# Kernel tuning notes

Hardware: AMD Instinct MI355X
Metric: run time of the kernel (lower is better)

The kernel has to match this reference:

```python
import jax, jax.numpy as jnp
import numpy as np

EMBED_DIM = 256
SEQ_LEN = 4096
BATCH = 8
ALPHA = 0.99


def setup_inputs() -> dict:
    key = jax.random.key(0)
    k_x, k_w, k_b = jax.random.split(key, 3)
    x = jax.random.normal(k_x, (BATCH, SEQ_LEN, EMBED_DIM), dtype=jnp.float32)
    # nn.Linear(embed_dim, 3*embed_dim): store as [d, 3d] so y = x @ Wqkv + bqkv
    Wqkv = jax.random.normal(k_w, (EMBED_DIM, 3 * EMBED_DIM), dtype=jnp.float32) * (EMBED_DIM ** -0.5)
    bqkv = jax.random.normal(k_b, (3 * EMBED_DIM,), dtype=jnp.float32) * 0.02
    return {"x": x, "Wqkv": Wqkv, "bqkv": bqkv}


def reference(x, Wqkv, bqkv):
    bs, sl, d = x.shape
    qkv = x @ Wqkv + bqkv                      # [bs, sl, 3d]
    q, k, v = jnp.split(qkv, 3, axis=-1)       # each [bs, sl, d]
    # causal * exponential-decay mask: M[i, j] = alpha**(i-j) for j <= i else 0
    i = jnp.arange(sl, dtype=jnp.float32)
    M = jnp.where(i[:, None] >= i[None, :],
                  jnp.power(jnp.float32(ALPHA), i[:, None] - i[None, :]),
                  0.0)                          # [sl, sl]
    scores = jnp.einsum('bqd,bkd->bqk', q, k) / jnp.sqrt(jnp.float32(d))
    out = jnp.einsum('bqk,bkd->bqd', scores * M, v)
    return out
```

## Files before the change

kernel.cpp:

```cpp
#include <hip/hip_runtime.h>

typedef __bf16 bf16x8 __attribute__((ext_vector_type(8)));
typedef float f32x4 __attribute__((ext_vector_type(4)));
typedef unsigned short u16;
typedef unsigned int u32;
typedef u16 u16x4 __attribute__((ext_vector_type(4)));
typedef u16 u16x8 __attribute__((ext_vector_type(8)));

#define L2ALPHA (-0.014499569f)

static __device__ __forceinline__ u16 f2bf(float f) {
    u32 u = __builtin_bit_cast(u32, f);
    return (u16)((u + 0x7FFFu + ((u >> 16) & 1u)) >> 16);
}

static __device__ __forceinline__ void gl2lds16(const void* g, void* l) {
    __builtin_amdgcn_global_load_lds(
        (const __attribute__((address_space(1))) u32*)g,
        (__attribute__((address_space(3))) u32*)l, 16, 0, 0);
}

__global__ __launch_bounds__(256, 2) void proj_kernel(
        const float* __restrict__ x, const float* __restrict__ Wq,
        const float* __restrict__ bias,
        u16* __restrict__ qb, u16* __restrict__ kb, u16* __restrict__ vb)
{
    __shared__ __align__(16) u16 Bs[32 * 128 * 8];
    __shared__ __align__(16) u16 As[4][32 * 40];

    const int tid = threadIdx.x, lane = tid & 63, w = tid >> 6;
    const int l = blockIdx.x;
    const int nb = l % 6;
    const int mt = l / 6;
    const int m0 = mt * 128, n0 = nb * 128;
    const int m = lane & 15, quad = lane >> 4;

    {
        const int col = tid & 127;
        const int khalf = tid >> 7;
        #pragma unroll
        for (int s = 0; s < 32; ++s) {
            int k0 = (khalf + 2 * s) * 4;
            u16x4 h;
            #pragma unroll
            for (int i = 0; i < 4; ++i)
                h[i] = f2bf(Wq[(k0 + i) * 768 + n0 + col]);
            *(u16x4*)&Bs[((k0 >> 3) * 128 + col) * 8 + (k0 & 7)] = h;
        }
    }
    __syncthreads();

    const int r = lane & 31, h = lane >> 5;
    const float* xrow = x + (size_t)(m0 + w * 32 + r) * 256 + h * 16;
    u16* As_w = &As[w][0];

    f32x4 acc[2][8];
    #pragma unroll
    for (int rt = 0; rt < 2; ++rt)
        #pragma unroll
        for (int ct = 0; ct < 8; ++ct)
            acc[rt][ct] = f32x4{0.f, 0.f, 0.f, 0.f};

    float4 g0 = *(const float4*)(xrow + 0);
    float4 g1 = *(const float4*)(xrow + 4);
    float4 g2 = *(const float4*)(xrow + 8);
    float4 g3 = *(const float4*)(xrow + 12);

    for (int kt = 0; kt < 8; ++kt) {
        u16x8 ha, hb;
        ha[0]=f2bf(g0.x); ha[1]=f2bf(g0.y); ha[2]=f2bf(g0.z); ha[3]=f2bf(g0.w);
        ha[4]=f2bf(g1.x); ha[5]=f2bf(g1.y); ha[6]=f2bf(g1.z); ha[7]=f2bf(g1.w);
        hb[0]=f2bf(g2.x); hb[1]=f2bf(g2.y); hb[2]=f2bf(g2.z); hb[3]=f2bf(g2.w);
        hb[4]=f2bf(g3.x); hb[5]=f2bf(g3.y); hb[6]=f2bf(g3.z); hb[7]=f2bf(g3.w);
        *(u16x8*)&As_w[r * 40 + h * 16]     = ha;
        *(u16x8*)&As_w[r * 40 + h * 16 + 8] = hb;

        if (kt < 7) {
            const float* xn = xrow + (kt + 1) * 32;
            g0 = *(const float4*)(xn + 0);
            g1 = *(const float4*)(xn + 4);
            g2 = *(const float4*)(xn + 8);
            g3 = *(const float4*)(xn + 12);
        }

        asm volatile("s_waitcnt lgkmcnt(0)" ::: "memory");

        bf16x8 af[2], bfr[8];
        #pragma unroll
        for (int rt = 0; rt < 2; ++rt)
            af[rt] = *(const bf16x8*)&As_w[(rt * 16 + m) * 40 + quad * 8];
        #pragma unroll
        for (int ct = 0; ct < 8; ++ct)
            bfr[ct] = *(const bf16x8*)&Bs[((kt * 4 + quad) * 128 + ct * 16 + m) * 8];
        #pragma unroll
        for (int rt = 0; rt < 2; ++rt)
            #pragma unroll
            for (int ct = 0; ct < 8; ++ct)
                acc[rt][ct] = __builtin_amdgcn_mfma_f32_16x16x32_bf16(
                    af[rt], bfr[ct], acc[rt][ct], 0, 0, 0);
    }

    const int b = m0 >> 12;
    const int jbase = (m0 & 4095) + w * 32;
    const int d0 = (nb & 1) * 128;

    if (nb < 2) {
        #pragma unroll
        for (int rt = 0; rt < 2; ++rt)
            #pragma unroll
            for (int ct = 0; ct < 8; ++ct) {
                int coll = ct * 16 + m;
                float bv = bias[d0 + coll];
                #pragma unroll
                for (int rr = 0; rr < 4; ++rr) {
                    int row = m0 + w * 32 + rt * 16 + quad * 4 + rr;
                    qb[(size_t)row * 256 + d0 + coll] = f2bf((acc[rt][ct][rr] + bv) * 0.0625f);
                }
            }
    } else if (nb < 4) {
        #pragma unroll
        for (int rt = 0; rt < 2; ++rt)
            #pragma unroll
            for (int ct = 0; ct < 8; ++ct) {
                int d = d0 + ct * 16 + m;
                float bv = bias[256 + d];
                int k8 = d >> 5, qk = (d >> 3) & 3, e = d & 7;
                #pragma unroll
                for (int rr = 0; rr < 4; ++rr) {
                    int j = jbase + rt * 16 + quad * 4 + rr;
                    int jt = j >> 5, hh = (j >> 4) & 1, mk = j & 15;
                    kb[((((size_t)(b * 128 + jt) * 2 + hh) * 8 + k8) * 64 + qk * 16 + mk) * 8 + e]
                        = f2bf(acc[rt][ct][rr] + bv);
                }
            }
    } else {
        #pragma unroll
        for (int rt = 0; rt < 2; ++rt)
            #pragma unroll
            for (int ct = 0; ct < 8; ++ct) {
                int d = d0 + ct * 16 + m;
                float bv = bias[512 + d];
                int dt = d >> 4, mv = d & 15;
                int j = jbase + rt * 16 + quad * 4;
                int jt = j >> 5, qv = (j >> 3) & 3, e0 = j & 7;
                u16x4 hv;
                #pragma unroll
                for (int rr = 0; rr < 4; ++rr) hv[rr] = f2bf(acc[rt][ct][rr] + bv);
                *(u16x4*)&vb[(((size_t)(b * 128 + jt) * 16 + dt) * 64 + qv * 16 + mv) * 8 + e0] = hv;
            }
    }
}

__global__ __launch_bounds__(256, 2) void attn_kernel(
        const u16* __restrict__ qb, const u16* __restrict__ kb,
        const u16* __restrict__ vb, float* __restrict__ out)
{
    __shared__ __align__(16) u16 Kf[2][8192];
    __shared__ __align__(16) u16 Vf[2][8192];
    __shared__ __align__(16) u16 Ps[4 * 32 * 40];

    const int tid = threadIdx.x, lane = tid & 63, w = tid >> 6;
    const int l = blockIdx.x;
    const int b = l & 7;
    const int m0 = (l >> 3) * 128;
    const int qrow0 = m0 + w * 32;
    const int m = lane & 15, quad = lane >> 4;
    const size_t rowbase = (size_t)b * 4096;

    bf16x8 qf[2][8];
    #pragma unroll
    for (int rg = 0; rg < 2; ++rg)
        #pragma unroll
        for (int k8 = 0; k8 < 8; ++k8)
            qf[rg][k8] = *(const bf16x8*)(qb + (rowbase + qrow0 + rg * 16 + m) * 256 + k8 * 32 + quad * 8);

    f32x4 acc[2][16];
    #pragma unroll
    for (int rg = 0; rg < 2; ++rg)
        #pragma unroll
        for (int dt = 0; dt < 16; ++dt)
            acc[rg][dt] = f32x4{0.f, 0.f, 0.f, 0.f};

    int t0 = (m0 - 1024) >> 5; if (t0 < 0) t0 = 0;
    const int t1 = (m0 >> 5) + 3;

    {
        const u16* kp = kb + (size_t)(b * 128 + t0) * 8192;
        const u16* vp = vb + (size_t)(b * 128 + t0) * 8192;
        #pragma unroll
        for (int s = 0; s < 4; ++s) {
            int c = tid + 256 * s;
            gl2lds16(kp + (size_t)c * 8, &Kf[0][c * 8]);
            gl2lds16(vp + (size_t)c * 8, &Vf[0][c * 8]);
        }
    }

    int p = 0;
    for (int t = t0; t <= t1; ++t) {
        __syncthreads();
        if (t < t1) {
            const u16* kp = kb + (size_t)(b * 128 + t + 1) * 8192;
            const u16* vp = vb + (size_t)(b * 128 + t + 1) * 8192;
            #pragma unroll
            for (int s = 0; s < 4; ++s) {
                int c = tid + 256 * s;
                gl2lds16(kp + (size_t)c * 8, &Kf[p ^ 1][c * 8]);
                gl2lds16(vp + (size_t)c * 8, &Vf[p ^ 1][c * 8]);
            }
        }
        const int j0 = t * 32;

        if (j0 <= qrow0 + 31 && j0 + 1055 >= qrow0) {
            f32x4 sA0{0.f,0.f,0.f,0.f}, sA1{0.f,0.f,0.f,0.f};
            f32x4 sB0{0.f,0.f,0.f,0.f}, sB1{0.f,0.f,0.f,0.f};
            #pragma unroll
            for (int k8 = 0; k8 < 8; ++k8) {
                bf16x8 bf0 = *(const bf16x8*)&Kf[p][(k8 * 64 + lane) * 8];
                sA0 = __builtin_amdgcn_mfma_f32_16x16x32_bf16(qf[0][k8], bf0, sA0, 0, 0, 0);
                sA1 = __builtin_amdgcn_mfma_f32_16x16x32_bf16(qf[1][k8], bf0, sA1, 0, 0, 0);
            }
            #pragma unroll
            for (int k8 = 0; k8 < 8; ++k8) {
                bf16x8 bf1 = *(const bf16x8*)&Kf[p][((8 + k8) * 64 + lane) * 8];
                sB0 = __builtin_amdgcn_mfma_f32_16x16x32_bf16(qf[0][k8], bf1, sB0, 0, 0, 0);
                sB1 = __builtin_amdgcn_mfma_f32_16x16x32_bf16(qf[1][k8], bf1, sB1, 0, 0, 0);
            }

            #pragma unroll
            for (int rg = 0; rg < 2; ++rg) {
                f32x4 sh0 = rg ? sA1 : sA0;
                f32x4 sh1 = rg ? sB1 : sB0;
                #pragma unroll
                for (int rr = 0; rr < 4; ++rr) {
                    int i = qrow0 + rg * 16 + quad * 4 + rr;
                    int dd0 = i - (j0 + m);
                    int dd1 = dd0 - 16;
                    float w0 = (dd0 >= 0) ? __builtin_amdgcn_exp2f((float)dd0 * L2ALPHA) : 0.0f;
                    float w1 = (dd1 >= 0) ? __builtin_amdgcn_exp2f((float)dd1 * L2ALPHA) : 0.0f;
                    int rowb = (w * 32 + rg * 16 + quad * 4 + rr) * 40;
                    Ps[rowb + m]      = f2bf(sh0[rr] * w0);
                    Ps[rowb + 16 + m] = f2bf(sh1[rr] * w1);
                }
            }
            asm volatile("s_waitcnt lgkmcnt(0)" ::: "memory");

            bf16x8 pa0 = *(const bf16x8*)&Ps[(w * 32 + m) * 40 + quad * 8];
            bf16x8 pa1 = *(const bf16x8*)&Ps[(w * 32 + 16 + m) * 40 + quad * 8];

            #pragma unroll
            for (int dt = 0; dt < 16; ++dt) {
                bf16x8 vf = *(const bf16x8*)&Vf[p][(dt * 64 + lane) * 8];
                acc[0][dt] = __builtin_amdgcn_mfma_f32_16x16x32_bf16(pa0, vf, acc[0][dt], 0, 0, 0);
                acc[1][dt] = __builtin_amdgcn_mfma_f32_16x16x32_bf16(pa1, vf, acc[1][dt], 0, 0, 0);
            }
        }
        p ^= 1;
    }

    #pragma unroll
    for (int rg = 0; rg < 2; ++rg)
        #pragma unroll
        for (int dt = 0; dt < 16; ++dt)
            #pragma unroll
            for (int rr = 0; rr < 4; ++rr)
                out[(rowbase + qrow0 + rg * 16 + quad * 4 + rr) * 256 + dt * 16 + m] = acc[rg][dt][rr];
}

extern "C" void kernel_launch(void* const* d_in, const int* in_sizes, int n_in,
                              void* d_out, int out_size, void* d_ws, size_t ws_size,
                              hipStream_t stream) {
    (void)in_sizes; (void)n_in; (void)out_size; (void)ws_size;
    const float* x    = (const float*)d_in[0];
    const float* Wq   = (const float*)d_in[1];
    const float* bias = (const float*)d_in[2];
    float* outp = (float*)d_out;

    const size_t per = (size_t)8 * 4096 * 256;
    u16* qb = (u16*)d_ws;
    u16* kb = qb + per;
    u16* vb = kb + per;

    proj_kernel<<<1536, 256, 0, stream>>>(x, Wq, bias, qb, kb, vb);
    attn_kernel<<<256, 256, 0, stream>>>(qb, kb, vb, outp);
}
```

Baseline: 197.0 us.

## Split KV tiles across two wave groups per block and reduce partial outputs

```diff
diff --git a/kernel.cpp b/kernel.cpp
--- a/kernel.cpp
+++ b/kernel.cpp
@@ -128,8 +128,8 @@
                 #pragma unroll
                 for (int rr = 0; rr < 4; ++rr) {
                     int j = jbase + rt * 16 + quad * 4 + rr;
-                    int jt = j >> 5, hh = (j >> 4) & 1, mk = j & 15;
-                    kb[((((size_t)(b * 128 + jt) * 2 + hh) * 8 + k8) * 64 + qk * 16 + mk) * 8 + e]
+                    int jt = j >> 5, jj = j & 31;
+                    kb[((((size_t)(b * 128 + jt) * 2 + (jj & 1)) * 8 + k8) * 64 + qk * 16 + (jj >> 1)) * 8 + e]
                         = f2bf(acc[rt][ct][rr] + bv);
                 }
             }
@@ -151,21 +151,22 @@
     }
 }
 
-__global__ __launch_bounds__(256, 2) void attn_kernel(
+__global__ __launch_bounds__(512, 2) void attn_kernel(
         const u16* __restrict__ qb, const u16* __restrict__ kb,
         const u16* __restrict__ vb, float* __restrict__ out)
 {
-    __shared__ __align__(16) u16 Kf[2][8192];
-    __shared__ __align__(16) u16 Vf[2][8192];
-    __shared__ __align__(16) u16 Ps[4 * 32 * 40];
+    __shared__ __align__(16) u16 KV[2][2][16384];
+    __shared__ __align__(16) u16 Ps[8 * 32 * 40];
 
     const int tid = threadIdx.x, lane = tid & 63, w = tid >> 6;
+    const int wp = w & 3, par = w >> 2;
     const int l = blockIdx.x;
     const int b = l & 7;
     const int m0 = (l >> 3) * 128;
-    const int qrow0 = m0 + w * 32;
+    const int qrow0 = m0 + wp * 32;
     const int m = lane & 15, quad = lane >> 4;
     const size_t rowbase = (size_t)b * 4096;
+    const size_t pbase = (size_t)b * 128;
 
     bf16x8 qf[2][8];
     #pragma unroll
@@ -183,45 +184,60 @@
 
     int t0 = (m0 - 1024) >> 5; if (t0 < 0) t0 = 0;
     const int t1 = (m0 >> 5) + 3;
+    const int nIter = (t1 - t0 + 2) >> 1;
 
     {
-        const u16* kp = kb + (size_t)(b * 128 + t0) * 8192;
-        const u16* vp = vb + (size_t)(b * 128 + t0) * 8192;
-        #pragma unroll
-        for (int s = 0; s < 4; ++s) {
-            int c = tid + 256 * s;
-            gl2lds16(kp + (size_t)c * 8, &Kf[0][c * 8]);
-            gl2lds16(vp + (size_t)c * 8, &Vf[0][c * 8]);
+        const u16* kpA = kb + (pbase + t0) * 8192;
+        const u16* vpA = vb + (pbase + t0) * 8192;
+        const u16* kpB = kpA + 8192;
+        const u16* vpB = vpA + 8192;
+        #pragma unroll
+        for (int s = 0; s < 2; ++s) {
+            int c = tid + 512 * s;
+            gl2lds16(kpA + (size_t)c * 8, &KV[0][0][c * 8]);
+            gl2lds16(vpA + (size_t)c * 8, &KV[0][0][8192 + c * 8]);
+            gl2lds16(kpB + (size_t)c * 8, &KV[0][1][c * 8]);
+            gl2lds16(vpB + (size_t)c * 8, &KV[0][1][8192 + c * 8]);
         }
     }
 
     int p = 0;
-    for (int t = t0; t <= t1; ++t) {
+    for (int it = 0; it < nIter; ++it) {
         __syncthreads();
-        if (t < t1) {
-            const u16* kp = kb + (size_t)(b * 128 + t + 1) * 8192;
-            const u16* vp = vb + (size_t)(b * 128 + t + 1) * 8192;
-            #pragma unroll
-            for (int s = 0; s < 4; ++s) {
-                int c = tid + 256 * s;
-                gl2lds16(kp + (size_t)c * 8, &Kf[p ^ 1][c * 8]);
-                gl2lds16(vp + (size_t)c * 8, &Vf[p ^ 1][c * 8]);
-            }
-        }
+        if (it + 1 < nIter) {
+            const int ta = t0 + 2 * (it + 1);
+            const bool haveB = (ta + 1 <= t1);
+            const u16* kpA = kb + (pbase + ta) * 8192;
+            const u16* vpA = vb + (pbase + ta) * 8192;
+            #pragma unroll
+            for (int s = 0; s < 2; ++s) {
+                int c = tid + 512 * s;
+                gl2lds16(kpA + (size_t)c * 8, &KV[p ^ 1][0][c * 8]);
+                gl2lds16(vpA + (size_t)c * 8, &KV[p ^ 1][0][8192 + c * 8]);
+                if (haveB) {
+                    gl2lds16(kpA + 8192 + (size_t)c * 8, &KV[p ^ 1][1][c * 8]);
+                    gl2lds16(vpA + 8192 + (size_t)c * 8, &KV[p ^ 1][1][8192 + c * 8]);
+                }
+            }
+        }
+
+        const int t = t0 + 2 * it + par;
         const int j0 = t * 32;
-
-        if (j0 <= qrow0 + 31 && j0 + 1055 >= qrow0) {
+        if (t <= t1 && j0 <= qrow0 + 31 && j0 + 1055 >= qrow0) {
+            const u16* Kt = &KV[p][par][0];
+            const u16* Vt = &KV[p][par][8192];
+
             f32x4 sA0{0.f,0.f,0.f,0.f}, sA1{0.f,0.f,0.f,0.f};
             f32x4 sB0{0.f,0.f,0.f,0.f}, sB1{0.f,0.f,0.f,0.f};
             #pragma unroll
             for (int k8 = 0; k8 < 8; ++k8) {
-                bf16x8 bf0 = *(const bf16x8*)&Kf[p][(k8 * 64 + lane) * 8];
+                bf16x8 bf0 = *(const bf16x8*)&Kt[(k8 * 64 + lane) * 8];
                 sA0 = __builtin_amdgcn_mfma_f32_16x16x32_bf16(qf[0][k8], bf0, sA0, 0, 0, 0);
                 sA1 = __builtin_amdgcn_mfma_f32_16x16x32_bf16(qf[1][k8], bf0, sA1, 0, 0, 0);
             }
             #pragma unroll
             for (int k8 = 0; k8 < 8; ++k8) {
-                bf16x8 bf1 = *(const bf16x8*)&Kf[p][((8 + k8) * 64 + lane) * 8];
+                bf16x8 bf1 = *(const bf16x8*)&Kt[((8 + k8) * 64 + lane) * 8];
                 sB0 = __builtin_amdgcn_mfma_f32_16x16x32_bf16(qf[0][k8], bf1, sB0, 0, 0, 0);
                 sB1 = __builtin_amdgcn_mfma_f32_16x16x32_bf16(qf[1][k8], bf1, sB1, 0, 0, 0);
             }
@@ -233,13 +249,13 @@
                 #pragma unroll
                 for (int rr = 0; rr < 4; ++rr) {
                     int i = qrow0 + rg * 16 + quad * 4 + rr;
-                    int dd0 = i - (j0 + m);
-                    int dd1 = dd0 - 16;
+                    int dd0 = i - (j0 + 2 * m);
+                    int dd1 = dd0 - 1;
                     float w0 = (dd0 >= 0) ? __builtin_amdgcn_exp2f((float)dd0 * L2ALPHA) : 0.0f;
                     float w1 = (dd1 >= 0) ? __builtin_amdgcn_exp2f((float)dd1 * L2ALPHA) : 0.0f;
                     int rowb = (w * 32 + rg * 16 + quad * 4 + rr) * 40;
-                    Ps[rowb + m]      = f2bf(sh0[rr] * w0);
-                    Ps[rowb + 16 + m] = f2bf(sh1[rr] * w1);
+                    u32 pv = (u32)f2bf(sh0[rr] * w0) | ((u32)f2bf(sh1[rr] * w1) << 16);
+                    *(u32*)&Ps[rowb + 2 * m] = pv;
                 }
             }
             asm volatile("s_waitcnt lgkmcnt(0)" ::: "memory");
@@ -249,7 +265,7 @@
 
             #pragma unroll
             for (int dt = 0; dt < 16; ++dt) {
-                bf16x8 vf = *(const bf16x8*)&Vf[p][(dt * 64 + lane) * 8];
+                bf16x8 vf = *(const bf16x8*)&Vt[(dt * 64 + lane) * 8];
                 acc[0][dt] = __builtin_amdgcn_mfma_f32_16x16x32_bf16(pa0, vf, acc[0][dt], 0, 0, 0);
                 acc[1][dt] = __builtin_amdgcn_mfma_f32_16x16x32_bf16(pa1, vf, acc[1][dt], 0, 0, 0);
             }
@@ -257,13 +273,29 @@
         p ^= 1;
     }
 
-    #pragma unroll
-    for (int rg = 0; rg < 2; ++rg)
-        #pragma unroll
-        for (int dt = 0; dt < 16; ++dt)
-            #pragma unroll
-            for (int rr = 0; rr < 4; ++rr)
-                out[(rowbase + qrow0 + rg * 16 + quad * 4 + rr) * 256 + dt * 16 + m] = acc[rg][dt][rr];
+    __syncthreads();
+    float* Comb = (float*)&KV[0][0][0];
+    if (par == 1) {
+        float* dst = Comb + (size_t)wp * 8192 + lane * 128;
+        #pragma unroll
+        for (int rg = 0; rg < 2; ++rg)
+            #pragma unroll
+            for (int dt = 0; dt < 16; ++dt)
+                *(f32x4*)(dst + (rg * 16 + dt) * 4) = acc[rg][dt];
+    }
+    __syncthreads();
+    if (par == 0) {
+        const float* src = Comb + (size_t)wp * 8192 + lane * 128;
+        #pragma unroll
+        for (int rg = 0; rg < 2; ++rg)
+            #pragma unroll
+            for (int dt = 0; dt < 16; ++dt) {
+                f32x4 o = acc[rg][dt] + *(const f32x4*)(src + (rg * 16 + dt) * 4);
+                #pragma unroll
+                for (int rr = 0; rr < 4; ++rr)
+                    out[(rowbase + qrow0 + rg * 16 + quad * 4 + rr) * 256 + dt * 16 + m] = o[rr];
+            }
+    }
 }
 
 extern "C" void kernel_launch(void* const* d_in, const int* in_sizes, int n_in,
@@ -281,5 +313,5 @@
     u16* vb = kb + per;
 
     proj_kernel<<<1536, 256, 0, stream>>>(x, Wq, bias, qb, kb, vb);
-    attn_kernel<<<256, 256, 0, stream>>>(qb, kb, vb, outp);
-}
+    attn_kernel<<<256, 512, 0, stream>>>(qb, kb, vb, outp);
+}
```

Result: faster. 177.8 us (-9.8%).
